# Kernel optimization log

Measured on AMD Instinct MI355X. Metric: run time of the kernel, lower is better.

## Reference

```python
import jax, jax.numpy as jnp
import numpy as np

N = 12288
IN_DIM = 128
OUT_DIM = 128
LR_SLOPE = 0.01
NEG_INF = -9e16


def setup_inputs() -> dict:
    key = jax.random.key(0)
    k1, k2, k3, k4 = jax.random.split(key, 4)
    emb_mat = jax.random.normal(k1, (N, IN_DIM), dtype=jnp.float32)
    adj_mat = jax.random.randint(k2, (N, N), 0, 2, dtype=jnp.int32)
    # xavier-normal-ish init for params
    W = jax.random.normal(k3, (OUT_DIM, IN_DIM), dtype=jnp.float32) * (2.0 / (IN_DIM + OUT_DIM)) ** 0.5
    a = jax.random.normal(k4, (2 * OUT_DIM, 1), dtype=jnp.float32) * (2.0 / (2 * OUT_DIM + 1)) ** 0.5
    return {"emb_mat": emb_mat, "adj_mat": adj_mat, "W": W, "a": a}


def reference(emb_mat, adj_mat, W, a):
    out_dim = W.shape[0]
    e_new = emb_mat @ W.T                       # [N, D_out]
    a1 = a[:out_dim, :]                         # [D_out, 1]
    a2 = a[out_dim:, :]                         # [D_out, 1]
    source_scores = e_new @ a1                  # [N, 1]
    target_scores = e_new @ a2                  # [N, 1]
    e = source_scores + target_scores.T         # [N, N] outer sum
    e = jax.nn.leaky_relu(e, negative_slope=LR_SLOPE)
    e = jnp.where(adj_mat > 0, e, NEG_INF)
    attention = jax.nn.softmax(e, axis=-1)      # [N, N]
    e_transf = attention @ e_new                # [N, D_out]
    return jax.nn.relu(e_transf)
```

## Files before the change

### kernel.cpp

```cpp
#include <hip/hip_runtime.h>


#define NN 12288
#define DIM 128
#define CSPLIT 8
#define COLS_PER (NN / CSPLIT)
#define BK 32
#define NCHUNK (COLS_PER / BK)

typedef __bf16 bf16x8 __attribute__((ext_vector_type(8)));
typedef float f32x4 __attribute__((ext_vector_type(4)));

__global__ __launch_bounds__(256) void k1_gemm(const float* __restrict__ emb,
                                               const float* __restrict__ W,
                                               const float* __restrict__ a,
                                               __bf16* __restrict__ Vt,
                                               float* __restrict__ s,
                                               float* __restrict__ t) {
  const int lane = threadIdx.x & 63;
  const int wave = threadIdx.x >> 6;
  const int m = lane & 15;
  const int quad = lane >> 4;
  const int row0 = blockIdx.x * 64 + wave * 16;

  f32x4 acc[8];
#pragma unroll
  for (int nb = 0; nb < 8; nb++) acc[nb] = (f32x4){0.f, 0.f, 0.f, 0.f};

#pragma unroll
  for (int ks = 0; ks < 4; ks++) {
    const int k0 = ks * 32 + quad * 8;
    const float* ep = emb + (size_t)(row0 + m) * DIM + k0;
    float4 lo = *(const float4*)ep;
    float4 hi = *(const float4*)(ep + 4);
    bf16x8 af = {(__bf16)lo.x, (__bf16)lo.y, (__bf16)lo.z, (__bf16)lo.w,
                 (__bf16)hi.x, (__bf16)hi.y, (__bf16)hi.z, (__bf16)hi.w};
#pragma unroll
    for (int nb = 0; nb < 8; nb++) {
      const float* wp = W + (size_t)(nb * 16 + m) * DIM + k0;
      float4 wlo = *(const float4*)wp;
      float4 whi = *(const float4*)(wp + 4);
      bf16x8 bf = {(__bf16)wlo.x, (__bf16)wlo.y, (__bf16)wlo.z, (__bf16)wlo.w,
                   (__bf16)whi.x, (__bf16)whi.y, (__bf16)whi.z, (__bf16)whi.w};
      acc[nb] = __builtin_amdgcn_mfma_f32_16x16x32_bf16(af, bf, acc[nb], 0, 0, 0);
    }
  }

  float a1v[8], a2v[8];
#pragma unroll
  for (int nb = 0; nb < 8; nb++) {
    a1v[nb] = a[nb * 16 + m];
    a2v[nb] = a[DIM + nb * 16 + m];
  }
#pragma unroll
  for (int r = 0; r < 4; r++) {
    const int gr = row0 + quad * 4 + r;
    float ps = 0.f, pt = 0.f;
#pragma unroll
    for (int nb = 0; nb < 8; nb++) {
      float e = acc[nb][r];
      ps += e * a1v[nb];
      pt += e * a2v[nb];
      Vt[(size_t)(nb * 16 + m) * NN + gr] = (__bf16)e;
    }
    ps += __shfl_xor(ps, 1); ps += __shfl_xor(ps, 2);
    ps += __shfl_xor(ps, 4); ps += __shfl_xor(ps, 8);
    pt += __shfl_xor(pt, 1); pt += __shfl_xor(pt, 2);
    pt += __shfl_xor(pt, 4); pt += __shfl_xor(pt, 8);
    if (m == 0) { s[gr] = ps; t[gr] = pt; }
  }
}

__global__ __launch_bounds__(256) void ktmax(const float* __restrict__ t,
                                             float* __restrict__ tmax) {
  __shared__ float red[256];
  float mx = -1e30f;
  for (int i = threadIdx.x; i < NN; i += 256) mx = fmaxf(mx, t[i]);
  red[threadIdx.x] = mx;
  __syncthreads();
  for (int off = 128; off; off >>= 1) {
    if ((int)threadIdx.x < off) red[threadIdx.x] = fmaxf(red[threadIdx.x], red[threadIdx.x + off]);
    __syncthreads();
  }
  if (threadIdx.x == 0) *tmax = red[0];
}

__global__ __launch_bounds__(256, 3) void k2_attn(const int* __restrict__ adj,
                                                  const __bf16* __restrict__ Vt,
                                                  const float* __restrict__ s,
                                                  const float* __restrict__ t,
                                                  const float* __restrict__ tmaxp,
                                                  float* __restrict__ part,
                                                  float* __restrict__ lpart) {
  __shared__ unsigned long long adjb[2][128][5];
  __shared__ __attribute__((aligned(16))) __bf16 vtb[2][128][40];

  const int tid = threadIdx.x;
  const int lane = tid & 63;
  const int wave = tid >> 6;
  const int m = lane & 15;
  const int quad = lane >> 4;
  const int row0 = blockIdx.x * 128;
  const int cs = blockIdx.y;
  const int col0 = cs * COLS_PER;
  const int rowA = row0 + wave * 32 + m;
  const int rowB = rowA + 16;

  const float Tmax = *tmaxp;
  const float sA = s[rowA], sB = s[rowB];
  const float uA = sA + Tmax, uB = sB + Tmax;
  const float mA = fmaxf(uA, 0.01f * uA);
  const float mB = fmaxf(uB, 0.01f * uB);

  f32x4 accA[8], accB[8];
#pragma unroll
  for (int nb = 0; nb < 8; nb++) {
    accA[nb] = (f32x4){0.f, 0.f, 0.f, 0.f};
    accB[nb] = (f32x4){0.f, 0.f, 0.f, 0.f};
  }
  float lA = 0.f, lB = 0.f;

  int4 ga[4];
  bf16x8 gv[2];
  const int fr = tid >> 3, fc = (tid & 7) * 4;
  const int vd = tid >> 2, vc = (tid & 3) * 8;

  auto fetch = [&](int c) {
    const int cc = col0 + c * BK;
#pragma unroll
    for (int p = 0; p < 4; p++)
      ga[p] = *(const int4*)(adj + (size_t)(row0 + fr + p * 32) * NN + cc + fc);
#pragma unroll
    for (int p = 0; p < 2; p++)
      gv[p] = *(const bf16x8*)(Vt + (size_t)(vd + p * 64) * NN + cc + vc);
  };
  auto commit = [&](int b) {
#pragma unroll
    for (int p = 0; p < 4; p++) {
      unsigned pk = (unsigned)(ga[p].x != 0) | ((unsigned)(ga[p].y != 0) << 8) |
                    ((unsigned)(ga[p].z != 0) << 16) | ((unsigned)(ga[p].w != 0) << 24);
      *(unsigned*)((unsigned char*)&adjb[b][fr + p * 32][0] + fc) = pk;
    }
#pragma unroll
    for (int p = 0; p < 2; p++)
      *(bf16x8*)&vtb[b][vd + p * 64][vc] = gv[p];
  };

  fetch(0);
  commit(0);
  __syncthreads();

  for (int c = 0; c < NCHUNK; c++) {
    if (c + 1 < NCHUNK) fetch(c + 1);

    const int b = c & 1;
    const float* tp = t + col0 + c * BK + quad * 8;
    float4 ct0 = *(const float4*)tp;
    float4 ct1 = *(const float4*)(tp + 4);
    unsigned long long avA = adjb[b][wave * 32 + m][quad];
    unsigned long long avB = adjb[b][wave * 32 + 16 + m][quad];

    bf16x8 pA, pB;
#define PEL(frag, jj, tv, av, ss, mm, ll)                               \
    {                                                                   \
      float v = (ss) + (tv);                                            \
      float lv = fmaxf(v, 0.01f * v);                                   \
      float e = (((av) >> (8 * (jj))) & 1) ? __expf(lv - (mm)) : 0.f;   \
      (ll) += e;                                                        \
      frag[jj] = (__bf16)e;                                             \
    }
    PEL(pA, 0, ct0.x, avA, sA, mA, lA)
    PEL(pA, 1, ct0.y, avA, sA, mA, lA)
    PEL(pA, 2, ct0.z, avA, sA, mA, lA)
    PEL(pA, 3, ct0.w, avA, sA, mA, lA)
    PEL(pA, 4, ct1.x, avA, sA, mA, lA)
    PEL(pA, 5, ct1.y, avA, sA, mA, lA)
    PEL(pA, 6, ct1.z, avA, sA, mA, lA)
    PEL(pA, 7, ct1.w, avA, sA, mA, lA)
    PEL(pB, 0, ct0.x, avB, sB, mB, lB)
    PEL(pB, 1, ct0.y, avB, sB, mB, lB)
    PEL(pB, 2, ct0.z, avB, sB, mB, lB)
    PEL(pB, 3, ct0.w, avB, sB, mB, lB)
    PEL(pB, 4, ct1.x, avB, sB, mB, lB)
    PEL(pB, 5, ct1.y, avB, sB, mB, lB)
    PEL(pB, 6, ct1.z, avB, sB, mB, lB)
    PEL(pB, 7, ct1.w, avB, sB, mB, lB)
#undef PEL

#pragma unroll
    for (int nb = 0; nb < 8; nb++) {
      bf16x8 bv = *(const bf16x8*)&vtb[b][nb * 16 + m][quad * 8];
      accA[nb] = __builtin_amdgcn_mfma_f32_16x16x32_bf16(pA, bv, accA[nb], 0, 0, 0);
      accB[nb] = __builtin_amdgcn_mfma_f32_16x16x32_bf16(pB, bv, accB[nb], 0, 0, 0);
    }

    if (c + 1 < NCHUNK) commit((c + 1) & 1);
    __syncthreads();
  }

  lA += __shfl_xor(lA, 16); lA += __shfl_xor(lA, 32);
  lB += __shfl_xor(lB, 16); lB += __shfl_xor(lB, 32);
  if (quad == 0) {
    lpart[(size_t)cs * NN + rowA] = lA;
    lpart[(size_t)cs * NN + rowB] = lB;
  }

  float* po = part + ((size_t)cs * NN + row0 + wave * 32) * DIM;
#pragma unroll
  for (int nb = 0; nb < 8; nb++) {
#pragma unroll
    for (int r = 0; r < 4; r++) {
      po[(size_t)(quad * 4 + r) * DIM + nb * 16 + m] = accA[nb][r];
      po[(size_t)(16 + quad * 4 + r) * DIM + nb * 16 + m] = accB[nb][r];
    }
  }
}

__global__ __launch_bounds__(256) void kl(const float* __restrict__ lpart,
                                          float* __restrict__ linv) {
  const int r = blockIdx.x * 256 + threadIdx.x;
  float l = 0.f;
#pragma unroll
  for (int cs = 0; cs < CSPLIT; cs++) l += lpart[(size_t)cs * NN + r];
  linv[r] = 1.0f / l;
}

__global__ __launch_bounds__(256) void k3_fin(const float* __restrict__ part,
                                              const float* __restrict__ linv,
                                              float* __restrict__ out) {
  const int idx = blockIdx.x * 256 + threadIdx.x;
  const int row = idx >> 5;
  const float4* p4 = (const float4*)part;
  float4 acc = p4[idx];
#pragma unroll
  for (int cs = 1; cs < CSPLIT; cs++) {
    float4 v = p4[(size_t)cs * (NN * DIM / 4) + idx];
    acc.x += v.x; acc.y += v.y; acc.z += v.z; acc.w += v.w;
  }
  const float li = linv[row];
  float4 o;
  o.x = fmaxf(acc.x * li, 0.f);
  o.y = fmaxf(acc.y * li, 0.f);
  o.z = fmaxf(acc.z * li, 0.f);
  o.w = fmaxf(acc.w * li, 0.f);
  ((float4*)out)[idx] = o;
}

extern "C" void kernel_launch(void* const* d_in, const int* in_sizes, int n_in,
                              void* d_out, int out_size, void* d_ws, size_t ws_size,
                              hipStream_t stream) {
  (void)in_sizes; (void)n_in; (void)out_size; (void)ws_size;
  const float* emb = (const float*)d_in[0];
  const int* adj = (const int*)d_in[1];
  const float* W = (const float*)d_in[2];
  const float* a = (const float*)d_in[3];
  float* out = (float*)d_out;

  char* ws = (char*)d_ws;
  __bf16* Vt = (__bf16*)ws;
  float* s = (float*)(ws + 3145728);
  float* t = (float*)(ws + 3194880);
  float* lpart = (float*)(ws + 3244032);
  float* linv = (float*)(ws + 3637248);
  float* tmax = (float*)(ws + 3686400);
  float* part = (float*)(ws + 3686656);

  k1_gemm<<<NN / 64, 256, 0, stream>>>(emb, W, a, Vt, s, t);
  ktmax<<<1, 256, 0, stream>>>(t, tmax);
  dim3 g2(NN / 128, CSPLIT);
  k2_attn<<<g2, 256, 0, stream>>>(adj, Vt, s, t, tmax, part, lpart);
  kl<<<NN / 256, 256, 0, stream>>>(lpart, linv);
  k3_fin<<<NN * DIM / 4 / 256, 256, 0, stream>>>(part, linv, out);
}
```

Before: 829.5 us.

## Stream adjacency directly to registers and DMA V tiles into LDS ring

The attention kernel stops staging adjacency through LDS bitmasks. Each lane now loads its own adjacency and target-score values straight into registers, double-buffered across two chunks. V tiles are copied into a 4-deep swizzled LDS ring with global_load_lds, using explicit vmcnt waits and raw barriers instead of a register commit plus __syncthreads. Scores are pre-scaled by log2(e) so exp2 replaces expf, the tmax reduction uses wave shuffles, and the row-sum inverse kernel is folded into the final reduction kernel. The hand-written waitcnt counts and the swizzle are fragile and could break correctness or ordering if the compiler reorders memory operations.

```diff
diff --git a/kernel.cpp b/kernel.cpp
--- a/kernel.cpp
+++ b/kernel.cpp
@@ -7,9 +7,16 @@
 #define COLS_PER (NN / CSPLIT)
 #define BK 32
 #define NCHUNK (COLS_PER / BK)
+#define LOG2E 1.4426950408889634f
 
 typedef __bf16 bf16x8 __attribute__((ext_vector_type(8)));
 typedef float f32x4 __attribute__((ext_vector_type(4)));
+
+__device__ __forceinline__ void gl_lds16(const __bf16* g, __bf16* l) {
+  __builtin_amdgcn_global_load_lds(
+      (const __attribute__((address_space(1))) void*)g,
+      (__attribute__((address_space(3))) void*)l, 16, 0, 0);
+}
 
 __global__ __launch_bounds__(256) void k1_gemm(const float* __restrict__ emb,
                                                const float* __restrict__ W,
@@ -67,33 +74,82 @@
     ps += __shfl_xor(ps, 4); ps += __shfl_xor(ps, 8);
     pt += __shfl_xor(pt, 1); pt += __shfl_xor(pt, 2);
     pt += __shfl_xor(pt, 4); pt += __shfl_xor(pt, 8);
-    if (m == 0) { s[gr] = ps; t[gr] = pt; }
+    if (m == 0) { s[gr] = ps * LOG2E; t[gr] = pt * LOG2E; }
   }
 }
 
 __global__ __launch_bounds__(256) void ktmax(const float* __restrict__ t,
                                              float* __restrict__ tmax) {
-  __shared__ float red[256];
-  float mx = -1e30f;
-  for (int i = threadIdx.x; i < NN; i += 256) mx = fmaxf(mx, t[i]);
-  red[threadIdx.x] = mx;
+  __shared__ float red[4];
+  const float4* t4 = (const float4*)t;
+  float mx = -3.0e38f;
+#pragma unroll
+  for (int i = 0; i < NN / 4 / 256; i++) {
+    float4 v = t4[i * 256 + threadIdx.x];
+    mx = fmaxf(mx, fmaxf(fmaxf(v.x, v.y), fmaxf(v.z, v.w)));
+  }
+#pragma unroll
+  for (int off = 1; off < 64; off <<= 1) mx = fmaxf(mx, __shfl_xor(mx, off));
+  if ((threadIdx.x & 63) == 0) red[threadIdx.x >> 6] = mx;
   __syncthreads();
-  for (int off = 128; off; off >>= 1) {
-    if ((int)threadIdx.x < off) red[threadIdx.x] = fmaxf(red[threadIdx.x], red[threadIdx.x + off]);
-    __syncthreads();
-  }
-  if (threadIdx.x == 0) *tmax = red[0];
-}
+  if (threadIdx.x == 0)
+    *tmax = fmaxf(fmaxf(red[0], red[1]), fmaxf(red[2], red[3]));
+}
+
+#define PELS(P, AA0, AA1, T0, T1, SS, MM, LL)                                   \
+  {                                                                             \
+    float v0 = SS + T0.x, v1 = SS + T0.y, v2 = SS + T0.z, v3 = SS + T0.w;       \
+    float v4 = SS + T1.x, v5 = SS + T1.y, v6 = SS + T1.z, v7 = SS + T1.w;       \
+    float e0 = (AA0.x != 0) ? __builtin_amdgcn_exp2f(fmaxf(v0, 0.01f * v0) - MM) : 0.f; \
+    float e1 = (AA0.y != 0) ? __builtin_amdgcn_exp2f(fmaxf(v1, 0.01f * v1) - MM) : 0.f; \
+    float e2 = (AA0.z != 0) ? __builtin_amdgcn_exp2f(fmaxf(v2, 0.01f * v2) - MM) : 0.f; \
+    float e3 = (AA0.w != 0) ? __builtin_amdgcn_exp2f(fmaxf(v3, 0.01f * v3) - MM) : 0.f; \
+    float e4 = (AA1.x != 0) ? __builtin_amdgcn_exp2f(fmaxf(v4, 0.01f * v4) - MM) : 0.f; \
+    float e5 = (AA1.y != 0) ? __builtin_amdgcn_exp2f(fmaxf(v5, 0.01f * v5) - MM) : 0.f; \
+    float e6 = (AA1.z != 0) ? __builtin_amdgcn_exp2f(fmaxf(v6, 0.01f * v6) - MM) : 0.f; \
+    float e7 = (AA1.w != 0) ? __builtin_amdgcn_exp2f(fmaxf(v7, 0.01f * v7) - MM) : 0.f; \
+    LL += ((e0 + e1) + (e2 + e3)) + ((e4 + e5) + (e6 + e7));                    \
+    P[0] = (__bf16)e0; P[1] = (__bf16)e1; P[2] = (__bf16)e2; P[3] = (__bf16)e3; \
+    P[4] = (__bf16)e4; P[5] = (__bf16)e5; P[6] = (__bf16)e6; P[7] = (__bf16)e7; \
+  }
+
+#define FETCH(cc, A0A, A1A, A0B, A1B, T0, T1)                                   \
+  {                                                                             \
+    const int off = (cc) * BK;                                                  \
+    A0A = *(const int4*)(abase + off); A1A = *(const int4*)(abase + off + 4);   \
+    A0B = *(const int4*)(bbase + off); A1B = *(const int4*)(bbase + off + 4);   \
+    T0 = *(const float4*)(tbase + off); T1 = *(const float4*)(tbase + off + 4); \
+  }
+
+#define DMA2(cc)                                                                \
+  {                                                                             \
+    __bf16* d = &vtb[(cc) & 3][dst0];                                           \
+    gl_lds16(vsrc0 + (size_t)(cc) * BK, d);                                     \
+    gl_lds16(vsrc1 + (size_t)(cc) * BK, d + 512);                               \
+  }
+
+#define COMPUTE(cc, A0A, A1A, A0B, A1B, T0, T1)                                 \
+  {                                                                             \
+    const __bf16* vb = &vtb[(cc) & 3][vread];                                   \
+    bf16x8 pA, pB;                                                              \
+    PELS(pA, A0A, A1A, T0, T1, sA, mA, lA)                                      \
+    PELS(pB, A0B, A1B, T0, T1, sB, mB, lB)                                      \
+    _Pragma("unroll")                                                           \
+    for (int nb = 0; nb < 8; nb++) {                                            \
+      bf16x8 bv = *(const bf16x8*)(vb + nb * 512);                              \
+      accA[nb] = __builtin_amdgcn_mfma_f32_16x16x32_bf16(pA, bv, accA[nb], 0, 0, 0); \
+      accB[nb] = __builtin_amdgcn_mfma_f32_16x16x32_bf16(pB, bv, accB[nb], 0, 0, 0); \
+    }                                                                           \
+  }
 
 __global__ __launch_bounds__(256, 3) void k2_attn(const int* __restrict__ adj,
                                                   const __bf16* __restrict__ Vt,
-                                                  const float* __restrict__ s,
-                                                  const float* __restrict__ t,
+                                                  const float* __restrict__ sK,
+                                                  const float* __restrict__ tK,
                                                   const float* __restrict__ tmaxp,
                                                   float* __restrict__ part,
                                                   float* __restrict__ lpart) {
-  __shared__ unsigned long long adjb[2][128][5];
-  __shared__ __attribute__((aligned(16))) __bf16 vtb[2][128][40];
+  __shared__ __attribute__((aligned(16))) __bf16 vtb[4][4096];
 
   const int tid = threadIdx.x;
   const int lane = tid & 63;
@@ -106,11 +162,23 @@
   const int rowA = row0 + wave * 32 + m;
   const int rowB = rowA + 16;
 
-  const float Tmax = *tmaxp;
-  const float sA = s[rowA], sB = s[rowB];
-  const float uA = sA + Tmax, uB = sB + Tmax;
+  const float TmaxK = *tmaxp;
+  const float sA = sK[rowA], sB = sK[rowB];
+  const float uA = sA + TmaxK, uB = sB + TmaxK;
   const float mA = fmaxf(uA, 0.01f * uA);
   const float mB = fmaxf(uB, 0.01f * uB);
+
+  const int p0 = wave * 128 + lane;
+  const int r0d = p0 >> 2;
+  const int cg0 = (p0 & 3) ^ ((r0d >> 1) & 3);
+  const __bf16* vsrc0 = Vt + (size_t)r0d * NN + col0 + cg0 * 8;
+  const __bf16* vsrc1 = vsrc0 + (size_t)16 * NN;
+  const int dst0 = wave * 1024;
+  const int vread = (m * 4 + (quad ^ ((m >> 1) & 3))) * 8;
+
+  const int* abase = adj + (size_t)rowA * NN + col0 + quad * 8;
+  const int* bbase = adj + (size_t)rowB * NN + col0 + quad * 8;
+  const float* tbase = tK + col0 + quad * 8;
 
   f32x4 accA[8], accB[8];
 #pragma unroll
@@ -120,82 +188,29 @@
   }
   float lA = 0.f, lB = 0.f;
 
-  int4 ga[4];
-  bf16x8 gv[2];
-  const int fr = tid >> 3, fc = (tid & 7) * 4;
-  const int vd = tid >> 2, vc = (tid & 3) * 8;
-
-  auto fetch = [&](int c) {
-    const int cc = col0 + c * BK;
-#pragma unroll
-    for (int p = 0; p < 4; p++)
-      ga[p] = *(const int4*)(adj + (size_t)(row0 + fr + p * 32) * NN + cc + fc);
-#pragma unroll
-    for (int p = 0; p < 2; p++)
-      gv[p] = *(const bf16x8*)(Vt + (size_t)(vd + p * 64) * NN + cc + vc);
-  };
-  auto commit = [&](int b) {
-#pragma unroll
-    for (int p = 0; p < 4; p++) {
-      unsigned pk = (unsigned)(ga[p].x != 0) | ((unsigned)(ga[p].y != 0) << 8) |
-                    ((unsigned)(ga[p].z != 0) << 16) | ((unsigned)(ga[p].w != 0) << 24);
-      *(unsigned*)((unsigned char*)&adjb[b][fr + p * 32][0] + fc) = pk;
-    }
-#pragma unroll
-    for (int p = 0; p < 2; p++)
-      *(bf16x8*)&vtb[b][vd + p * 64][vc] = gv[p];
-  };
-
-  fetch(0);
-  commit(0);
-  __syncthreads();
-
-  for (int c = 0; c < NCHUNK; c++) {
-    if (c + 1 < NCHUNK) fetch(c + 1);
-
-    const int b = c & 1;
-    const float* tp = t + col0 + c * BK + quad * 8;
-    float4 ct0 = *(const float4*)tp;
-    float4 ct1 = *(const float4*)(tp + 4);
-    unsigned long long avA = adjb[b][wave * 32 + m][quad];
-    unsigned long long avB = adjb[b][wave * 32 + 16 + m][quad];
-
-    bf16x8 pA, pB;
-#define PEL(frag, jj, tv, av, ss, mm, ll)                               \
-    {                                                                   \
-      float v = (ss) + (tv);                                            \
-      float lv = fmaxf(v, 0.01f * v);                                   \
-      float e = (((av) >> (8 * (jj))) & 1) ? __expf(lv - (mm)) : 0.f;   \
-      (ll) += e;                                                        \
-      frag[jj] = (__bf16)e;                                             \
-    }
-    PEL(pA, 0, ct0.x, avA, sA, mA, lA)
-    PEL(pA, 1, ct0.y, avA, sA, mA, lA)
-    PEL(pA, 2, ct0.z, avA, sA, mA, lA)
-    PEL(pA, 3, ct0.w, avA, sA, mA, lA)
-    PEL(pA, 4, ct1.x, avA, sA, mA, lA)
-    PEL(pA, 5, ct1.y, avA, sA, mA, lA)
-    PEL(pA, 6, ct1.z, avA, sA, mA, lA)
-    PEL(pA, 7, ct1.w, avA, sA, mA, lA)
-    PEL(pB, 0, ct0.x, avB, sB, mB, lB)
-    PEL(pB, 1, ct0.y, avB, sB, mB, lB)
-    PEL(pB, 2, ct0.z, avB, sB, mB, lB)
-    PEL(pB, 3, ct0.w, avB, sB, mB, lB)
-    PEL(pB, 4, ct1.x, avB, sB, mB, lB)
-    PEL(pB, 5, ct1.y, avB, sB, mB, lB)
-    PEL(pB, 6, ct1.z, avB, sB, mB, lB)
-    PEL(pB, 7, ct1.w, avB, sB, mB, lB)
-#undef PEL
-
-#pragma unroll
-    for (int nb = 0; nb < 8; nb++) {
-      bf16x8 bv = *(const bf16x8*)&vtb[b][nb * 16 + m][quad * 8];
-      accA[nb] = __builtin_amdgcn_mfma_f32_16x16x32_bf16(pA, bv, accA[nb], 0, 0, 0);
-      accB[nb] = __builtin_amdgcn_mfma_f32_16x16x32_bf16(pB, bv, accB[nb], 0, 0, 0);
-    }
-
-    if (c + 1 < NCHUNK) commit((c + 1) & 1);
-    __syncthreads();
+  int4 xA0, xA1, xB0, xB1; float4 xT0, xT1;
+  int4 yA0, yA1, yB0, yB1; float4 yT0, yT1;
+
+  DMA2(0);
+  DMA2(1);
+  FETCH(0, xA0, xA1, xB0, xB1, xT0, xT1);
+  asm volatile("s_waitcnt vmcnt(0)" ::: "memory");
+  __builtin_amdgcn_s_barrier();
+
+  for (int c = 0; c < NCHUNK; c += 2) {
+    if (c + 2 < NCHUNK) DMA2(c + 2);
+    FETCH(c + 1, yA0, yA1, yB0, yB1, yT0, yT1);
+    COMPUTE(c, xA0, xA1, xB0, xB1, xT0, xT1);
+    asm volatile("s_waitcnt vmcnt(4)" ::: "memory");
+    __builtin_amdgcn_s_barrier();
+
+    if (c + 3 < NCHUNK) DMA2(c + 3);
+    if (c + 2 < NCHUNK) FETCH(c + 2, xA0, xA1, xB0, xB1, xT0, xT1);
+    COMPUTE(c + 1, yA0, yA1, yB0, yB1, yT0, yT1);
+    if (c + 2 < NCHUNK) {
+      asm volatile("s_waitcnt vmcnt(4)" ::: "memory");
+      __builtin_amdgcn_s_barrier();
+    }
   }
 
   lA += __shfl_xor(lA, 16); lA += __shfl_xor(lA, 32);
@@ -216,33 +231,33 @@
   }
 }
 
-__global__ __launch_bounds__(256) void kl(const float* __restrict__ lpart,
-                                          float* __restrict__ linv) {
-  const int r = blockIdx.x * 256 + threadIdx.x;
-  float l = 0.f;
-#pragma unroll
-  for (int cs = 0; cs < CSPLIT; cs++) l += lpart[(size_t)cs * NN + r];
-  linv[r] = 1.0f / l;
-}
-
 __global__ __launch_bounds__(256) void k3_fin(const float* __restrict__ part,
-                                              const float* __restrict__ linv,
+                                              const float* __restrict__ lpart,
                                               float* __restrict__ out) {
-  const int idx = blockIdx.x * 256 + threadIdx.x;
-  const int row = idx >> 5;
+  __shared__ float li[8];
+  const int base = blockIdx.x * 256;
+  const int idx = base + (int)threadIdx.x;
+  if (threadIdx.x < 8) {
+    const int r = (base >> 5) + (int)threadIdx.x;
+    float l = 0.f;
+#pragma unroll
+    for (int c2 = 0; c2 < CSPLIT; c2++) l += lpart[(size_t)c2 * NN + r];
+    li[threadIdx.x] = 1.0f / l;
+  }
   const float4* p4 = (const float4*)part;
   float4 acc = p4[idx];
 #pragma unroll
-  for (int cs = 1; cs < CSPLIT; cs++) {
-    float4 v = p4[(size_t)cs * (NN * DIM / 4) + idx];
+  for (int c2 = 1; c2 < CSPLIT; c2++) {
+    float4 v = p4[(size_t)c2 * (NN * DIM / 4) + idx];
     acc.x += v.x; acc.y += v.y; acc.z += v.z; acc.w += v.w;
   }
-  const float li = linv[row];
+  __syncthreads();
+  const float liv = li[threadIdx.x >> 5];
   float4 o;
-  o.x = fmaxf(acc.x * li, 0.f);
-  o.y = fmaxf(acc.y * li, 0.f);
-  o.z = fmaxf(acc.z * li, 0.f);
-  o.w = fmaxf(acc.w * li, 0.f);
+  o.x = fmaxf(acc.x * liv, 0.f);
+  o.y = fmaxf(acc.y * liv, 0.f);
+  o.z = fmaxf(acc.z * liv, 0.f);
+  o.w = fmaxf(acc.w * liv, 0.f);
   ((float4*)out)[idx] = o;
 }
 
@@ -261,7 +276,6 @@
   float* s = (float*)(ws + 3145728);
   float* t = (float*)(ws + 3194880);
   float* lpart = (float*)(ws + 3244032);
-  float* linv = (float*)(ws + 3637248);
   float* tmax = (float*)(ws + 3686400);
   float* part = (float*)(ws + 3686656);
 
@@ -269,6 +283,5 @@
   ktmax<<<1, 256, 0, stream>>>(t, tmax);
   dim3 g2(NN / 128, CSPLIT);
   k2_attn<<<g2, 256, 0, stream>>>(adj, Vt, s, t, tmax, part, lpart);
-  kl<<<NN / 256, 256, 0, stream>>>(lpart, linv);
-  k3_fin<<<NN * DIM / 4 / 256, 256, 0, stream>>>(part, linv, out);
-}
+  k3_fin<<<NN * DIM / 4 / 256, 256, 0, stream>>>(part, lpart, out);
+}
```

Result: no change. 832.8 us (+0.4%).
